# Kernel tuning notes

Measured on AMD Instinct MI355X. Metric: run time of the kernel, lower is better.

The kernel has to match this reference:

```python
import jax, jax.numpy as jnp
import numpy as np

B, S, D = 2, 2048, 1024
H, HD = 16, 64          # num_heads, head_dim = D // H
W = 31                  # window_size (odd)
E = 1024                # embed_dim


def setup_inputs() -> dict:
    key = jax.random.key(0)
    ks = jax.random.split(key, 12)
    sd = 1.0 / np.sqrt(D)
    so = 1.0 / np.sqrt(H * HD)
    return {
        "x": jax.random.normal(ks[0], (B, S, D), jnp.float32),
        "fsq": jax.random.normal(ks[1], (1, S, D), jnp.float32),   # feature_squeeze_token
        "pos": jax.random.normal(ks[2], (1, S, D), jnp.float32),   # position_token
        "Wq": jax.random.normal(ks[3], (H, D, HD), jnp.float32) * sd,
        "bq": jax.random.normal(ks[4], (H, HD), jnp.float32) * sd,
        "Wk": jax.random.normal(ks[5], (H, D, HD), jnp.float32) * sd,
        "bk": jax.random.normal(ks[6], (H, HD), jnp.float32) * sd,
        "Wv": jax.random.normal(ks[7], (H, D, HD), jnp.float32) * sd,
        "bv": jax.random.normal(ks[8], (H, HD), jnp.float32) * sd,
        "Wo": jax.random.normal(ks[9], (H * HD, E), jnp.float32) * so,
        "bo": jax.random.normal(ks[10], (E,), jnp.float32) * so,
    }


def reference(x, fsq, pos, Wq, bq, Wk, bk, Wv, bv, Wo, bo):
    b, s, d = x.shape
    pad = (W - 1) // 2
    # sliding windows: (B, S, W, D), zero-padded at sequence edges
    xp = jnp.pad(x, ((0, 0), (pad, pad), (0, 0)))
    idx = jnp.arange(s)[:, None] + jnp.arange(W)[None, :]  # (S, W)
    win = xp[:, idx, :]  # (B, S, W, D)
    a = jnp.broadcast_to(fsq[:, :, None, :], (b, s, 1, d))  # squeeze token per pos
    bt = jnp.broadcast_to(pos[:, :, None, :], (b, s, 1, d))  # position token per pos
    kv = jnp.concatenate([win, bt, a], axis=2)  # (B, S, K=W+2, D)
    q = jnp.broadcast_to(fsq, (b, s, d))        # query = squeeze token
    # per-head projections (heads stacked on axis h)
    qh = jnp.einsum("bsd,hde->bhse", q, Wq) + bq[None, :, None, :]        # (B,H,S,HD)
    kh = jnp.einsum("bskd,hde->bhske", kv, Wk) + bk[None, :, None, None, :]
    vh = jnp.einsum("bskd,hde->bhske", kv, Wv) + bv[None, :, None, None, :]
    scores = jnp.einsum("bhse,bhske->bhsk", qh, kh) / jnp.sqrt(jnp.asarray(HD, x.dtype))
    attn = jax.nn.softmax(scores, axis=-1)  # dropout is identity in eval
    outh = jnp.einsum("bhsk,bhske->bhse", attn, vh)  # (B,H,S,HD)
    concat = outh.transpose(0, 2, 1, 3).reshape(b, s, H * HD)  # heads concat order 0..H-1
    return concat @ Wo + bo  # (B, S, E)
```

## Files before the change

### kernel.cpp

```cpp
#include <hip/hip_runtime.h>


typedef __attribute__((ext_vector_type(8))) short bf16x8;
typedef __attribute__((ext_vector_type(4))) float f32x4;
typedef unsigned short u16;
typedef unsigned int u32;

__device__ __forceinline__ float bf2f(u16 u) {
  union { u32 i; float f; } v; v.i = ((u32)u) << 16; return v.f;
}
__device__ __forceinline__ u16 f2bf(float f) {
  union { float f; u32 i; } v; v.f = f;
  u32 r = v.i + 0x7fffu + ((v.i >> 16) & 1u);
  return (u16)(r >> 16);
}
__device__ __forceinline__ float2 unpk(u32 u) {
  union { u32 i; float f; } lo, hi;
  lo.i = u << 16; hi.i = u & 0xffff0000u;
  return make_float2(lo.f, hi.f);
}
__device__ __forceinline__ float dot8(uint4 a, uint4 b) {
  float s = 0.f;
  { float2 x = unpk(a.x), y = unpk(b.x); s += x.x*y.x + x.y*y.y; }
  { float2 x = unpk(a.y), y = unpk(b.y); s += x.x*y.x + x.y*y.y; }
  { float2 x = unpk(a.z), y = unpk(b.z); s += x.x*y.x + x.y*y.y; }
  { float2 x = unpk(a.w), y = unpk(b.w); s += x.x*y.x + x.y*y.y; }
  return s;
}
__device__ __forceinline__ void gload_lds16(const u16* g, u16* l) {
  __builtin_amdgcn_global_load_lds((const __attribute__((address_space(1))) void*)(g),
                                   (__attribute__((address_space(3))) void*)(l),
                                   16, 0, 0);
}
__device__ __forceinline__ uint4 pack8(float4 a, float4 b) {
  union { u16 h[8]; uint4 q; } u;
  u.h[0] = f2bf(a.x); u.h[1] = f2bf(a.y); u.h[2] = f2bf(a.z); u.h[3] = f2bf(a.w);
  u.h[4] = f2bf(b.x); u.h[5] = f2bf(b.y); u.h[6] = f2bf(b.z); u.h[7] = f2bf(b.w);
  return u.q;
}

__device__ __forceinline__ void transpose_body(const float* src, u16* dst,
                                               int R, int C, int r0, int c0) {
  __shared__ u16 tile[64][72];
  int t = threadIdx.x;
#pragma unroll
  for (int i = 0; i < 16; ++i) {
    int idx = i * 256 + t;
    int r = idx >> 6, c = idx & 63;
    tile[r][c] = f2bf(src[(size_t)(r0 + r) * C + (c0 + c)]);
  }
  __syncthreads();
#pragma unroll
  for (int i = 0; i < 16; ++i) {
    int idx = i * 256 + t;
    int c = idx >> 6, r = idx & 63;
    dst[(size_t)(c0 + c) * R + (r0 + r)] = tile[r][c];
  }
}

__global__ __launch_bounds__(256) void prep(const float* __restrict__ x,
                                            const float* __restrict__ fsq,
                                            const float* __restrict__ pos,
                                            const float* __restrict__ Wq,
                                            const float* __restrict__ Wk,
                                            const float* __restrict__ Wv,
                                            const float* __restrict__ Wo,
                                            u16* __restrict__ xb,
                                            u16* __restrict__ fsqb,
                                            u16* __restrict__ posb,
                                            u16* __restrict__ WqT,
                                            u16* __restrict__ WkT,
                                            u16* __restrict__ WvT,
                                            u16* __restrict__ WoT) {
  int bid = blockIdx.x;
  if (bid < 4096) {
    int i = bid * 256 + threadIdx.x;
    const float* src; u16* dst; int off;
    if (i < 524288)      { src = x;   dst = xb;   off = i; }
    else if (i < 786432) { src = fsq; dst = fsqb; off = i - 524288; }
    else                 { src = pos; dst = posb; off = i - 786432; }
    float4 a = ((const float4*)src)[2 * off];
    float4 b = ((const float4*)src)[2 * off + 1];
    ((uint4*)dst)[off] = pack8(a, b);
  } else {
    int id = bid - 4096;
    int z = id >> 8, rest = id & 255;
    int xx = rest & 15, yy = rest >> 4;
    if (z < 3) {
      const float* s = (z == 0) ? Wq : (z == 1) ? Wk : Wv;
      u16* d = (z == 0) ? WqT : (z == 1) ? WkT : WvT;
      size_t off = (size_t)xx * 65536;
      transpose_body(s + off, d + off, 1024, 64, yy * 64, 0);
    } else {
      transpose_body(Wo, WoT, 1024, 1024, yy * 64, xx * 64);
    }
  }
}

__device__ __forceinline__ int swz(int R, int c) {
  return (R * 8 + (c ^ (R & 7))) * 8;
}

template <int MT, bool OUTF32>
__device__ __forceinline__ void gemm_body(const u16* __restrict__ Ap,
                                          const u16* __restrict__ BT,
                                          const float* __restrict__ bias,
                                          void* Cp, int tile_n) {
  __shared__ u16 As[MT * 32 * 64];
  __shared__ u16 Bs[128 * 64];
  const int t = threadIdx.x, lane = t & 63, wave = t >> 6;
  const int wm = (wave >> 1) * (MT * 16), wn = (wave & 1) * 64;
  const int row16 = lane & 15, quad = lane >> 4;
  const int l8 = lane >> 3;
  const int cswz = (lane & 7) ^ l8;

  f32x4 acc[MT][4] = {};

  for (int k0 = 0; k0 < 1024; k0 += 64) {
    __syncthreads();
#pragma unroll
    for (int j = 0; j < MT; ++j) {
      int r = wave * (MT * 8) + j * 8 + l8;
      gload_lds16(Ap + (size_t)r * 1024 + k0 + cswz * 8,
                  &As[wave * (MT * 512) + j * 512]);
    }
#pragma unroll
    for (int j = 0; j < 4; ++j) {
      int r = wave * 32 + j * 8 + l8;
      gload_lds16(BT + (size_t)(tile_n + r) * 1024 + k0 + cswz * 8,
                  &Bs[wave * 2048 + j * 512]);
    }
    __syncthreads();

#pragma unroll
    for (int kb = 0; kb < 2; ++kb) {
      bf16x8 a_frag[MT], b_frag[4];
#pragma unroll
      for (int i = 0; i < MT; ++i)
        a_frag[i] = *(const bf16x8*)&As[swz(wm + i * 16 + row16, kb * 4 + quad)];
#pragma unroll
      for (int j = 0; j < 4; ++j)
        b_frag[j] = *(const bf16x8*)&Bs[swz(wn + j * 16 + row16, kb * 4 + quad)];
#pragma unroll
      for (int i = 0; i < MT; ++i)
#pragma unroll
        for (int j = 0; j < 4; ++j)
          acc[i][j] = __builtin_amdgcn_mfma_f32_16x16x32_bf16(
              a_frag[i], b_frag[j], acc[i][j], 0, 0, 0);
    }
  }

#pragma unroll
  for (int j = 0; j < 4; ++j) {
    int n = tile_n + wn + j * 16 + row16;
    float bb = bias[n];
#pragma unroll
    for (int i = 0; i < MT; ++i) {
      int m0 = wm + i * 16 + quad * 4;
#pragma unroll
      for (int r = 0; r < 4; ++r) {
        float val = acc[i][j][r] + bb;
        if (OUTF32) ((float*)Cp)[(size_t)(m0 + r) * 1024 + n] = val;
        else        ((u16*)Cp)[(size_t)(m0 + r) * 1024 + n] = f2bf(val);
      }
    }
  }
}

__global__ __launch_bounds__(256) void proj_gemm(const u16* __restrict__ xb,
                                                 const u16* __restrict__ fsqb,
                                                 const u16* __restrict__ posb,
                                                 const u16* __restrict__ WkT,
                                                 const u16* __restrict__ WvT,
                                                 const u16* __restrict__ WqT,
                                                 const float* __restrict__ bk,
                                                 const float* __restrict__ bv,
                                                 const float* __restrict__ bq,
                                                 u16* __restrict__ Kp,
                                                 u16* __restrict__ Vp,
                                                 u16* __restrict__ Qp) {
  int bid = blockIdx.x;
  const u16* Ap; const u16* BT; const float* bias; u16* C; int tile_n;
  if (bid < 1024) {
    int tm = bid >> 4, tn = bid & 15;
    if (tm < 32)      Ap = xb   + (size_t)tm * 128 * 1024;
    else if (tm < 48) Ap = fsqb + (size_t)(tm - 32) * 128 * 1024;
    else              Ap = posb + (size_t)(tm - 48) * 128 * 1024;
    if (tn < 8) { BT = WkT; bias = bk; C = Kp + (size_t)tm * 128 * 1024; tile_n = tn * 128; }
    else        { BT = WvT; bias = bv; C = Vp + (size_t)tm * 128 * 1024; tile_n = (tn - 8) * 128; }
  } else {
    int q = bid - 1024; int tm = q >> 3; tile_n = (q & 7) * 128;
    Ap = fsqb + (size_t)tm * 128 * 1024; BT = WqT; bias = bq;
    C = Qp + (size_t)tm * 128 * 1024;
  }
  gemm_body<4, false>(Ap, BT, bias, C, tile_n);
}

__global__ __launch_bounds__(256) void out_gemm(const u16* __restrict__ Att,
                                                const u16* __restrict__ WoT,
                                                const float* __restrict__ bo,
                                                float* __restrict__ Out) {
  int tile_n = blockIdx.x * 128, tm = blockIdx.y;
  gemm_body<2, true>(Att + (size_t)tm * 64 * 1024, WoT, bo,
                     Out + (size_t)tm * 64 * 1024, tile_n);
}

#define AST 72
#define QS  0
#define KWS 2304
#define VTS 6912
#define KPS 11520
#define KFS 13824
#define SMT 16128

__global__ __launch_bounds__(256) void attn_tile(const u16* __restrict__ Qp,
                                                 const u16* __restrict__ Kp,
                                                 const u16* __restrict__ Vp,
                                                 const float* __restrict__ bk,
                                                 const float* __restrict__ bv,
                                                 u16* __restrict__ Att) {
  __shared__ u16 sm[SMT];
  __shared__ float smP[32 * 36];

  const int t = threadIdx.x;
  const int bid = blockIdx.x;
  const int s0 = (bid & 63) * 32;
  const int h  = (bid >> 6) & 15;
  const int b  = bid >> 10;
  const int lane = t & 63, wave = t >> 6;
  const int row16 = lane & 15, quad = lane >> 4;
  const int hcol = h * 64;

  { int w = t >> 3, oct = t & 7;
    *(uint4*)&sm[QS + w * AST + oct * 8] =
        *(const uint4*)(Qp + (size_t)(s0 + w) * 1024 + hcol + oct * 8); }
#pragma unroll
  for (int i = 0; i < 2; ++i) {
    int task = i * 256 + t; int w = task >> 3, oct = task & 7;
    int g = s0 + w - 15;
    uint4 v;
    if ((unsigned)g < 2048u)
      v = *(const uint4*)(Kp + (size_t)(b * 2048 + g) * 1024 + hcol + oct * 8);
    else
      v = pack8(*(const float4*)(bk + hcol + oct * 8),
                *(const float4*)(bk + hcol + oct * 8 + 4));
    *(uint4*)&sm[KWS + w * AST + oct * 8] = v;
  }
#pragma unroll
  for (int i = 0; i < 2; ++i) {
    int task = i * 256 + t;
    int r = (task >> 3) & 31, oct = task & 7;
    size_t grow = (i == 0) ? (size_t)(6144 + s0 + r) : (size_t)(4096 + s0 + r);
    *(uint4*)&sm[(i == 0 ? KPS : KFS) + r * AST + oct * 8] =
        *(const uint4*)(Kp + grow * 1024 + hcol + oct * 8);
  }
#pragma unroll
  for (int i = 0; i < 2; ++i) {
    int task = i * 256 + t; int w = task >> 3, oct = task & 7;
    int g = s0 + w - 15;
    union { u16 h8[8]; uint4 q; } u;
    if ((unsigned)g < 2048u)
      u.q = *(const uint4*)(Vp + (size_t)(b * 2048 + g) * 1024 + hcol + oct * 8);
    else
      u.q = pack8(*(const float4*)(bv + hcol + oct * 8),
                  *(const float4*)(bv + hcol + oct * 8 + 4));
#pragma unroll
    for (int j = 0; j < 8; ++j)
      sm[VTS + (oct * 8 + j) * AST + w] = u.h8[j];
  }
  __syncthreads();

  {
    f32x4 accS[2] = {};
#pragma unroll
    for (int kc = 0; kc < 2; ++kc) {
      bf16x8 bf_ = *(const bf16x8*)&sm[KWS + (wave * 16 + row16) * AST + kc * 32 + quad * 8];
#pragma unroll
      for (int mi = 0; mi < 2; ++mi) {
        bf16x8 af = *(const bf16x8*)&sm[QS + (mi * 16 + row16) * AST + kc * 32 + quad * 8];
        accS[mi] = __builtin_amdgcn_mfma_f32_16x16x32_bf16(af, bf_, accS[mi], 0, 0, 0);
      }
    }
#pragma unroll
    for (int mi = 0; mi < 2; ++mi)
#pragma unroll
      for (int r = 0; r < 4; ++r) {
        int s = mi * 16 + quad * 4 + r;
        int w = wave * 16 + row16;
        int d = w - s;
        if (d >= 0 && d <= 30) smP[s * 36 + d] = accS[mi][r] * 0.125f;
      }
  }
  if (t < 64) {
    int s = t >> 1, which = t & 1;
    int base = (which == 0) ? KPS : KFS;
    float a = 0.f;
#pragma unroll
    for (int c = 0; c < 8; ++c)
      a += dot8(*(const uint4*)&sm[QS + s * AST + c * 8],
                *(const uint4*)&sm[base + s * AST + c * 8]);
    smP[s * 36 + 31 + which] = a * 0.125f;
  }
  __syncthreads();

  if (t < 32) {
    int s = t;
    float vals[33];
#pragma unroll
    for (int k = 0; k < 33; ++k) vals[k] = smP[s * 36 + k];
    float mx = -1e30f;
#pragma unroll
    for (int k = 0; k < 33; ++k) mx = fmaxf(mx, vals[k]);
    float sum = 0.f;
#pragma unroll
    for (int k = 0; k < 33; ++k) { vals[k] = __expf(vals[k] - mx); sum += vals[k]; }
    float inv = 1.f / sum;
    u32* prow = (u32*)&sm[QS + s * AST];
#pragma unroll
    for (int j = 0; j < 32; ++j) prow[j] = 0;
#pragma unroll
    for (int k = 0; k < 31; ++k)
      sm[QS + s * AST + s + k] = f2bf(vals[k] * inv);
    smP[s * 36 + 33] = vals[31] * inv;
    smP[s * 36 + 34] = vals[32] * inv;
  }
  __syncthreads();

  {
    f32x4 accO[2] = {};
#pragma unroll
    for (int kc = 0; kc < 2; ++kc) {
      bf16x8 bf_ = *(const bf16x8*)&sm[VTS + (wave * 16 + row16) * AST + kc * 32 + quad * 8];
#pragma unroll
      for (int mi = 0; mi < 2; ++mi) {
        bf16x8 af = *(const bf16x8*)&sm[QS + (mi * 16 + row16) * AST + kc * 32 + quad * 8];
        accO[mi] = __builtin_amdgcn_mfma_f32_16x16x32_bf16(af, bf_, accO[mi], 0, 0, 0);
      }
    }
#pragma unroll
    for (int mi = 0; mi < 2; ++mi)
#pragma unroll
      for (int r = 0; r < 4; ++r) {
        int s = mi * 16 + quad * 4 + r;
        int e = wave * 16 + row16;
        float o = accO[mi][r]
                + smP[s * 36 + 33] * bf2f(Vp[(size_t)(6144 + s0 + s) * 1024 + hcol + e])
                + smP[s * 36 + 34] * bf2f(Vp[(size_t)(4096 + s0 + s) * 1024 + hcol + e]);
        Att[(size_t)(b * 2048 + s0 + s) * 1024 + hcol + e] = f2bf(o);
      }
  }
}

extern "C" void kernel_launch(void* const* d_in, const int* in_sizes, int n_in,
                              void* d_out, int out_size, void* d_ws, size_t ws_size,
                              hipStream_t stream) {
  (void)in_sizes; (void)n_in; (void)out_size; (void)ws_size;

  const float* x   = (const float*)d_in[0];
  const float* fsq = (const float*)d_in[1];
  const float* pos = (const float*)d_in[2];
  const float* Wq  = (const float*)d_in[3];
  const float* bq  = (const float*)d_in[4];
  const float* Wk  = (const float*)d_in[5];
  const float* bk  = (const float*)d_in[6];
  const float* Wv  = (const float*)d_in[7];
  const float* bv  = (const float*)d_in[8];
  const float* Wo  = (const float*)d_in[9];
  const float* bo  = (const float*)d_in[10];

  u16* ws = (u16*)d_ws;
  const size_t M1 = 1024 * 1024;
  u16* WqT  = ws + 0 * M1;
  u16* WkT  = ws + 1 * M1;
  u16* WvT  = ws + 2 * M1;
  u16* WoT  = ws + 3 * M1;
  u16* Qp   = ws + 4 * M1;
  u16* Kp   = ws + 6 * M1;
  u16* Vp   = ws + 14 * M1;
  u16* fsqb = ws + 22 * M1;
  u16* posb = ws + 24 * M1;
  u16* xb   = ws + 26 * M1;
  u16* Att  = ws + 22 * M1;

  prep<<<5120, 256, 0, stream>>>(x, fsq, pos, Wq, Wk, Wv, Wo,
                                 xb, fsqb, posb, WqT, WkT, WvT, WoT);

  proj_gemm<<<1152, 256, 0, stream>>>(xb, fsqb, posb, WkT, WvT, WqT,
                                      bk, bv, bq, Kp, Vp, Qp);

  attn_tile<<<2048, 256, 0, stream>>>(Qp, Kp, Vp, bk, bv, Att);

  out_gemm<<<dim3(8, 64), 256, 0, stream>>>(Att, WoT, bo, (float*)d_out);
}
```

Measured before the change: 198.9 us.

## Store V projection transposed and load attention windows via direct LDS DMA

The V projection GEMM now writes its output transposed (feature-major, 8-byte packed stores), so the attention kernel can load the V window already transposed. Interior tiles stage K and V windows with direct global-to-LDS loads into unpadded 64-wide rows, using a 32-row window shifted by one; only boundary tiles keep the masked, bias-filled path. The proj and out GEMM block indices are remapped so tiles sharing an A row-block land on the same XCD, for L2 reuse. This removes the per-element scalar LDS transpose of V but adds strided transposed global writes in the projection and possible LDS bank conflicts from dropping the padding.

Measured after the change: 202.5 us. Within noise of the previous version (+1.8%).

```diff
diff --git a/kernel.cpp b/kernel.cpp
--- a/kernel.cpp
+++ b/kernel.cpp
@@ -5,6 +5,7 @@
 typedef __attribute__((ext_vector_type(4))) float f32x4;
 typedef unsigned short u16;
 typedef unsigned int u32;
+typedef unsigned long long u64;
 
 __device__ __forceinline__ float bf2f(u16 u) {
   union { u32 i; float f; } v; v.i = ((u32)u) << 16; return v.f;
@@ -101,11 +102,11 @@
   return (R * 8 + (c ^ (R & 7))) * 8;
 }
 
-template <int MT, bool OUTF32>
+template <int MT, int OMODE>
 __device__ __forceinline__ void gemm_body(const u16* __restrict__ Ap,
                                           const u16* __restrict__ BT,
                                           const float* __restrict__ bias,
-                                          void* Cp, int tile_n) {
+                                          void* Cp, int tile_n, int tile_m) {
   __shared__ u16 As[MT * 32 * 64];
   __shared__ u16 Bs[128 * 64];
   const int t = threadIdx.x, lane = t & 63, wave = t >> 6;
@@ -157,11 +158,18 @@
 #pragma unroll
     for (int i = 0; i < MT; ++i) {
       int m0 = wm + i * 16 + quad * 4;
-#pragma unroll
-      for (int r = 0; r < 4; ++r) {
-        float val = acc[i][j][r] + bb;
-        if (OUTF32) ((float*)Cp)[(size_t)(m0 + r) * 1024 + n] = val;
-        else        ((u16*)Cp)[(size_t)(m0 + r) * 1024 + n] = f2bf(val);
+      if (OMODE == 2) {
+        union { u16 h[4]; u64 q; } o;
+#pragma unroll
+        for (int r = 0; r < 4; ++r) o.h[r] = f2bf(acc[i][j][r] + bb);
+        *(u64*)((u16*)Cp + (size_t)n * 8192 + tile_m + m0) = o.q;
+      } else {
+#pragma unroll
+        for (int r = 0; r < 4; ++r) {
+          float val = acc[i][j][r] + bb;
+          if (OMODE == 1) ((float*)Cp)[(size_t)(m0 + r) * 1024 + n] = val;
+          else            ((u16*)Cp)[(size_t)(m0 + r) * 1024 + n] = f2bf(val);
+        }
       }
     }
   }
@@ -177,45 +185,51 @@
                                                  const float* __restrict__ bv,
                                                  const float* __restrict__ bq,
                                                  u16* __restrict__ Kp,
-                                                 u16* __restrict__ Vp,
+                                                 u16* __restrict__ VpT,
                                                  u16* __restrict__ Qp) {
   int bid = blockIdx.x;
-  const u16* Ap; const u16* BT; const float* bias; u16* C; int tile_n;
   if (bid < 1024) {
-    int tm = bid >> 4, tn = bid & 15;
+    int xcd = bid & 7, i = bid >> 3;
+    int tm = xcd * 8 + (i & 7);
+    int tn = i >> 3;
+    const u16* Ap;
     if (tm < 32)      Ap = xb   + (size_t)tm * 128 * 1024;
     else if (tm < 48) Ap = fsqb + (size_t)(tm - 32) * 128 * 1024;
     else              Ap = posb + (size_t)(tm - 48) * 128 * 1024;
-    if (tn < 8) { BT = WkT; bias = bk; C = Kp + (size_t)tm * 128 * 1024; tile_n = tn * 128; }
-    else        { BT = WvT; bias = bv; C = Vp + (size_t)tm * 128 * 1024; tile_n = (tn - 8) * 128; }
+    if (tn < 8)
+      gemm_body<4, 0>(Ap, WkT, bk, Kp + (size_t)tm * 128 * 1024, tn * 128, 0);
+    else
+      gemm_body<4, 2>(Ap, WvT, bv, VpT, (tn - 8) * 128, tm * 128);
   } else {
-    int q = bid - 1024; int tm = q >> 3; tile_n = (q & 7) * 128;
-    Ap = fsqb + (size_t)tm * 128 * 1024; BT = WqT; bias = bq;
-    C = Qp + (size_t)tm * 128 * 1024;
-  }
-  gemm_body<4, false>(Ap, BT, bias, C, tile_n);
+    int qb = bid - 1024;
+    int tn = qb & 7, tm = qb >> 3;
+    gemm_body<4, 0>(fsqb + (size_t)tm * 128 * 1024, WqT, bq,
+                    Qp + (size_t)tm * 128 * 1024, tn * 128, 0);
+  }
 }
 
 __global__ __launch_bounds__(256) void out_gemm(const u16* __restrict__ Att,
                                                 const u16* __restrict__ WoT,
                                                 const float* __restrict__ bo,
                                                 float* __restrict__ Out) {
-  int tile_n = blockIdx.x * 128, tm = blockIdx.y;
-  gemm_body<2, true>(Att + (size_t)tm * 64 * 1024, WoT, bo,
-                     Out + (size_t)tm * 64 * 1024, tile_n);
-}
-
-#define AST 72
-#define QS  0
-#define KWS 2304
-#define VTS 6912
-#define KPS 11520
-#define KFS 13824
-#define SMT 16128
+  int bid = blockIdx.x;
+  int xcd = bid & 7, idx = bid >> 3;
+  int tm = xcd * 8 + (idx & 7);
+  int tile_n = (idx >> 3) * 128;
+  gemm_body<2, 1>(Att + (size_t)tm * 64 * 1024, WoT, bo,
+                  Out + (size_t)tm * 64 * 1024, tile_n, 0);
+}
+
+#define QS   0
+#define KPS  2304
+#define KFS  4608
+#define KWS  6912
+#define VTS  11008
+#define SMT  15104
 
 __global__ __launch_bounds__(256) void attn_tile(const u16* __restrict__ Qp,
                                                  const u16* __restrict__ Kp,
-                                                 const u16* __restrict__ Vp,
+                                                 const u16* __restrict__ VpT,
                                                  const float* __restrict__ bk,
                                                  const float* __restrict__ bv,
                                                  u16* __restrict__ Att) {
@@ -232,41 +246,52 @@
   const int hcol = h * 64;
 
   { int w = t >> 3, oct = t & 7;
-    *(uint4*)&sm[QS + w * AST + oct * 8] =
+    *(uint4*)&sm[QS + w * 72 + oct * 8] =
         *(const uint4*)(Qp + (size_t)(s0 + w) * 1024 + hcol + oct * 8); }
-#pragma unroll
-  for (int i = 0; i < 2; ++i) {
-    int task = i * 256 + t; int w = task >> 3, oct = task & 7;
-    int g = s0 + w - 15;
-    uint4 v;
-    if ((unsigned)g < 2048u)
-      v = *(const uint4*)(Kp + (size_t)(b * 2048 + g) * 1024 + hcol + oct * 8);
-    else
-      v = pack8(*(const float4*)(bk + hcol + oct * 8),
-                *(const float4*)(bk + hcol + oct * 8 + 4));
-    *(uint4*)&sm[KWS + w * AST + oct * 8] = v;
-  }
-#pragma unroll
-  for (int i = 0; i < 2; ++i) {
-    int task = i * 256 + t;
-    int r = (task >> 3) & 31, oct = task & 7;
-    size_t grow = (i == 0) ? (size_t)(6144 + s0 + r) : (size_t)(4096 + s0 + r);
-    *(uint4*)&sm[(i == 0 ? KPS : KFS) + r * AST + oct * 8] =
-        *(const uint4*)(Kp + grow * 1024 + hcol + oct * 8);
-  }
-#pragma unroll
-  for (int i = 0; i < 2; ++i) {
-    int task = i * 256 + t; int w = task >> 3, oct = task & 7;
-    int g = s0 + w - 15;
-    union { u16 h8[8]; uint4 q; } u;
-    if ((unsigned)g < 2048u)
-      u.q = *(const uint4*)(Vp + (size_t)(b * 2048 + g) * 1024 + hcol + oct * 8);
-    else
-      u.q = pack8(*(const float4*)(bv + hcol + oct * 8),
-                  *(const float4*)(bv + hcol + oct * 8 + 4));
-#pragma unroll
-    for (int j = 0; j < 8; ++j)
-      sm[VTS + (oct * 8 + j) * AST + w] = u.h8[j];
+  { int r = t >> 3, oct = t & 7;
+    *(uint4*)&sm[KPS + r * 72 + oct * 8] =
+        *(const uint4*)(Kp + (size_t)(6144 + s0 + r) * 1024 + hcol + oct * 8);
+    *(uint4*)&sm[KFS + r * 72 + oct * 8] =
+        *(const uint4*)(Kp + (size_t)(4096 + s0 + r) * 1024 + hcol + oct * 8); }
+
+  const bool boundary = (s0 == 0) || (s0 == 2016);
+  if (!boundary) {
+#pragma unroll
+    for (int i = 0; i < 2; ++i) {
+      int task = i * 256 + t;
+      int w = task >> 3, oct = task & 7;
+      gload_lds16(Kp + (size_t)(b * 2048 + s0 + w - 16) * 1024 + hcol + oct * 8,
+                  &sm[KWS + (i * 256 + wave * 64) * 8]);
+      int e = w;
+      gload_lds16(VpT + (size_t)(hcol + e) * 8192 + (b * 2048 + s0 - 16) + oct * 8,
+                  &sm[VTS + (i * 256 + wave * 64) * 8]);
+    }
+  } else {
+#pragma unroll
+    for (int i = 0; i < 2; ++i) {
+      int task = i * 256 + t;
+      int w = task >> 3, oct = task & 7;
+      int g = s0 + w - 16;
+      uint4 kv;
+      if ((unsigned)g < 2048u)
+        kv = *(const uint4*)(Kp + (size_t)(b * 2048 + g) * 1024 + hcol + oct * 8);
+      else
+        kv = pack8(*(const float4*)(bk + hcol + oct * 8),
+                   *(const float4*)(bk + hcol + oct * 8 + 4));
+      *(uint4*)&sm[KWS + w * 64 + oct * 8] = kv;
+
+      int e = w;
+      int g0 = s0 + oct * 8 - 16;
+      uint4 vv;
+      if (g0 >= 0 && g0 + 7 < 2048)
+        vv = *(const uint4*)(VpT + (size_t)(hcol + e) * 8192 + (b * 2048 + g0));
+      else {
+        u16 hb = f2bf(bv[hcol + e]);
+        u32 pp = (u32)hb | ((u32)hb << 16);
+        vv = make_uint4(pp, pp, pp, pp);
+      }
+      *(uint4*)&sm[VTS + e * 64 + oct * 8] = vv;
+    }
   }
   __syncthreads();
 
@@ -274,10 +299,10 @@
     f32x4 accS[2] = {};
 #pragma unroll
     for (int kc = 0; kc < 2; ++kc) {
-      bf16x8 bf_ = *(const bf16x8*)&sm[KWS + (wave * 16 + row16) * AST + kc * 32 + quad * 8];
+      bf16x8 bf_ = *(const bf16x8*)&sm[KWS + (wave * 16 + row16) * 64 + kc * 32 + quad * 8];
 #pragma unroll
       for (int mi = 0; mi < 2; ++mi) {
-        bf16x8 af = *(const bf16x8*)&sm[QS + (mi * 16 + row16) * AST + kc * 32 + quad * 8];
+        bf16x8 af = *(const bf16x8*)&sm[QS + (mi * 16 + row16) * 72 + kc * 32 + quad * 8];
         accS[mi] = __builtin_amdgcn_mfma_f32_16x16x32_bf16(af, bf_, accS[mi], 0, 0, 0);
       }
     }
@@ -288,7 +313,7 @@
         int s = mi * 16 + quad * 4 + r;
         int w = wave * 16 + row16;
         int d = w - s;
-        if (d >= 0 && d <= 30) smP[s * 36 + d] = accS[mi][r] * 0.125f;
+        if (d >= 1 && d <= 31) smP[s * 36 + d - 1] = accS[mi][r] * 0.125f;
       }
   }
   if (t < 64) {
@@ -297,8 +322,8 @@
     float a = 0.f;
 #pragma unroll
     for (int c = 0; c < 8; ++c)
-      a += dot8(*(const uint4*)&sm[QS + s * AST + c * 8],
-                *(const uint4*)&sm[base + s * AST + c * 8]);
+      a += dot8(*(const uint4*)&sm[QS + s * 72 + c * 8],
+                *(const uint4*)&sm[base + s * 72 + c * 8]);
     smP[s * 36 + 31 + which] = a * 0.125f;
   }
   __syncthreads();
@@ -315,12 +340,12 @@
 #pragma unroll
     for (int k = 0; k < 33; ++k) { vals[k] = __expf(vals[k] - mx); sum += vals[k]; }
     float inv = 1.f / sum;
-    u32* prow = (u32*)&sm[QS + s * AST];
+    u32* prow = (u32*)&sm[QS + s * 72];
 #pragma unroll
     for (int j = 0; j < 32; ++j) prow[j] = 0;
 #pragma unroll
     for (int k = 0; k < 31; ++k)
-      sm[QS + s * AST + s + k] = f2bf(vals[k] * inv);
+      sm[QS + s * 72 + (s + 1 + k)] = f2bf(vals[k] * inv);
     smP[s * 36 + 33] = vals[31] * inv;
     smP[s * 36 + 34] = vals[32] * inv;
   }
@@ -330,10 +355,10 @@
     f32x4 accO[2] = {};
 #pragma unroll
     for (int kc = 0; kc < 2; ++kc) {
-      bf16x8 bf_ = *(const bf16x8*)&sm[VTS + (wave * 16 + row16) * AST + kc * 32 + quad * 8];
+      bf16x8 bf_ = *(const bf16x8*)&sm[VTS + (wave * 16 + row16) * 64 + kc * 32 + quad * 8];
 #pragma unroll
       for (int mi = 0; mi < 2; ++mi) {
-        bf16x8 af = *(const bf16x8*)&sm[QS + (mi * 16 + row16) * AST + kc * 32 + quad * 8];
+        bf16x8 af = *(const bf16x8*)&sm[QS + (mi * 16 + row16) * 72 + kc * 32 + quad * 8];
         accO[mi] = __builtin_amdgcn_mfma_f32_16x16x32_bf16(af, bf_, accO[mi], 0, 0, 0);
       }
     }
@@ -344,8 +369,8 @@
         int s = mi * 16 + quad * 4 + r;
         int e = wave * 16 + row16;
         float o = accO[mi][r]
-                + smP[s * 36 + 33] * bf2f(Vp[(size_t)(6144 + s0 + s) * 1024 + hcol + e])
-                + smP[s * 36 + 34] * bf2f(Vp[(size_t)(4096 + s0 + s) * 1024 + hcol + e]);
+                + smP[s * 36 + 33] * bf2f(VpT[(size_t)(hcol + e) * 8192 + 6144 + s0 + s])
+                + smP[s * 36 + 34] * bf2f(VpT[(size_t)(hcol + e) * 8192 + 4096 + s0 + s]);
         Att[(size_t)(b * 2048 + s0 + s) * 1024 + hcol + e] = f2bf(o);
       }
   }
@@ -376,7 +401,7 @@
   u16* WoT  = ws + 3 * M1;
   u16* Qp   = ws + 4 * M1;
   u16* Kp   = ws + 6 * M1;
-  u16* Vp   = ws + 14 * M1;
+  u16* VpT  = ws + 14 * M1;
   u16* fsqb = ws + 22 * M1;
   u16* posb = ws + 24 * M1;
   u16* xb   = ws + 26 * M1;
@@ -386,9 +411,9 @@
                                  xb, fsqb, posb, WqT, WkT, WvT, WoT);
 
   proj_gemm<<<1152, 256, 0, stream>>>(xb, fsqb, posb, WkT, WvT, WqT,
-                                      bk, bv, bq, Kp, Vp, Qp);
-
-  attn_tile<<<2048, 256, 0, stream>>>(Qp, Kp, Vp, bk, bv, Att);
-
-  out_gemm<<<dim3(8, 64), 256, 0, stream>>>(Att, WoT, bo, (float*)d_out);
-}
+                                      bk, bv, bq, Kp, VpT, Qp);
+
+  attn_tile<<<2048, 256, 0, stream>>>(Qp, Kp, VpT, bk, bv, Att);
+
+  out_gemm<<<512, 256, 0, stream>>>(Att, WoT, bo, (float*)d_out);
+}
```
